# Kernel tuning notes

Hardware: AMD Instinct MI355X
Metric: run time of the kernel (lower is better)

## Reference

```python
import jax, jax.numpy as jnp
import numpy as np

N_NODES = 100000
N_EDGES = 640000
NIN = 128
NOUT = 128


def setup_inputs() -> dict:
    key = jax.random.key(0)
    ks = jax.random.split(key, 10)
    scale = 1.0 / np.sqrt(NIN)
    x = jax.random.normal(ks[0], (N_NODES, NIN), dtype=jnp.float32)
    edge_index = jax.random.randint(ks[1], (2, N_EDGES), 0, N_NODES, dtype=jnp.int64)
    edge_attr = jnp.zeros((N_EDGES, 1), dtype=jnp.float32)
    Wk = jax.random.uniform(ks[2], (NIN, NOUT), jnp.float32, -scale, scale)
    bk = jax.random.uniform(ks[3], (NOUT,), jnp.float32, -scale, scale)
    Wq = jax.random.uniform(ks[4], (NIN, NOUT), jnp.float32, -scale, scale)
    bq = jax.random.uniform(ks[5], (NOUT,), jnp.float32, -scale, scale)
    Wv = jax.random.uniform(ks[6], (NIN, NOUT), jnp.float32, -scale, scale)
    bv = jax.random.uniform(ks[7], (NOUT,), jnp.float32, -scale, scale)
    Wskip = jax.random.uniform(ks[8], (NIN, NOUT), jnp.float32, -scale, scale)
    bias = jax.random.uniform(ks[9], (NOUT,), jnp.float32, -scale, scale)
    return {
        "x": x, "edge_index": edge_index, "edge_attr": edge_attr,
        "Wk": Wk, "bk": bk, "Wq": Wq, "bq": bq,
        "Wv": Wv, "bv": bv, "Wskip": Wskip, "bias": bias,
    }


def reference(x, edge_index, edge_attr, Wk, bk, Wq, bq, Wv, bv, Wskip, bias):
    # PyG ResGatedGraphConv: out_i = W_skip x_i + b + sum_{j->i} sigmoid(k_i + q_j) * v_j
    # k = lin_key(x) (applied to dst), q = lin_query(x) (src), v = lin_value(x) (src)
    src, dst = edge_index[0], edge_index[1]
    k = x @ Wk + bk            # [N, NOUT]
    q = x @ Wq + bq            # [N, NOUT]
    v = x @ Wv + bv            # [N, NOUT]
    eta = jax.nn.sigmoid(k[dst] + q[src])   # [E, NOUT] per-edge gate
    msg = eta * v[src]                       # [E, NOUT]
    agg = jax.ops.segment_sum(msg, dst, num_segments=x.shape[0])  # [N, NOUT]
    return agg + x @ Wskip + bias
```

## Files before the change

### kernel.cpp

```cpp
#include <hip/hip_runtime.h>
#include <hip/hip_bf16.h>

typedef __bf16 v4bf __attribute__((ext_vector_type(4)));
typedef __bf16 v8bf __attribute__((ext_vector_type(8)));
typedef float  v16f __attribute__((ext_vector_type(16)));
typedef float  f4v  __attribute__((ext_vector_type(4)));
typedef unsigned int u4v __attribute__((ext_vector_type(4)));

#define LOG2E 1.44269504088896340736f

__device__ __forceinline__ unsigned short f2bf(float f) {
    union { float f; unsigned int u; } a; a.f = f;
    unsigned int r = a.u + 0x7FFFu + ((a.u >> 16) & 1u);
    return (unsigned short)(r >> 16);
}

__device__ __forceinline__ void unpack8v(u4v w, float* f) {
    #pragma unroll
    for (int i = 0; i < 4; ++i) {
        f[2 * i]     = __uint_as_float(w[i] << 16);
        f[2 * i + 1] = __uint_as_float(w[i] & 0xFFFF0000u);
    }
}

__global__ __launch_bounds__(256) void prep_w_zero(
    const float* __restrict__ Wk, const float* __restrict__ Wq,
    const float* __restrict__ Wv, const float* __restrict__ Ws,
    unsigned short* __restrict__ Wt, int* __restrict__ deg, int N)
{
    int i = blockIdx.x * 256 + threadIdx.x;
    if (i < 65536) {
        int m = i >> 14;
        int r = i & 16383;
        int n = r >> 7, k = r & 127;
        const float* W = (m == 0) ? Wk : (m == 1) ? Wq : (m == 2) ? Wv : Ws;
        float scale = (m == 0) ? -LOG2E : (m == 1) ? LOG2E : 1.0f;
        Wt[i] = f2bf(W[k * 128 + n] * scale);
    }
    if (i < N) deg[i] = 0;
}

__global__ __launch_bounds__(1024, 4) void gemm_fused(
    const float* __restrict__ x, int N,
    const unsigned short* __restrict__ Wt,
    const float* __restrict__ bk, const float* __restrict__ bq,
    const float* __restrict__ bv, const float* __restrict__ bs,
    unsigned short* __restrict__ kws, unsigned short* __restrict__ qv,
    float* __restrict__ out,
    const int* __restrict__ ei, int E,
    int* __restrict__ deg, int* __restrict__ pos)
{
    for (int e = blockIdx.x * 1024 + threadIdx.x; e < E; e += gridDim.x * 1024) {
        pos[e] = atomicAdd(&deg[ei[E + e]], 1);
    }

    __shared__ __align__(16) unsigned short xs[128 * 132];
    const int t  = threadIdx.x;
    const int tb = blockIdx.x * 128;

    {
        const int srow = t >> 3;
        const int scol = (t & 7) << 4;
        const int gr = tb + srow;
        float4 f0, f1, f2, f3;
        if (gr < N) {
            const float* xp = x + (size_t)gr * 128 + scol;
            f0 = *(const float4*)(xp);
            f1 = *(const float4*)(xp + 4);
            f2 = *(const float4*)(xp + 8);
            f3 = *(const float4*)(xp + 12);
        } else {
            f0 = f1 = f2 = f3 = make_float4(0.f, 0.f, 0.f, 0.f);
        }
        unsigned short* sp = xs + srow * 132 + scol;
        ushort4 p;
        p.x = f2bf(f0.x); p.y = f2bf(f0.y); p.z = f2bf(f0.z); p.w = f2bf(f0.w);
        *(ushort4*)(sp) = p;
        p.x = f2bf(f1.x); p.y = f2bf(f1.y); p.z = f2bf(f1.z); p.w = f2bf(f1.w);
        *(ushort4*)(sp + 4) = p;
        p.x = f2bf(f2.x); p.y = f2bf(f2.y); p.z = f2bf(f2.z); p.w = f2bf(f2.w);
        *(ushort4*)(sp + 8) = p;
        p.x = f2bf(f3.x); p.y = f2bf(f3.y); p.z = f2bf(f3.z); p.w = f2bf(f3.w);
        *(ushort4*)(sp + 12) = p;
    }

    const int wid = t >> 6;
    const int m   = wid >> 2;
    const int ct  = wid & 3;
    const int l   = t & 63;
    const int lr  = l & 31;
    const int h   = l >> 5;
    const int kb  = h * 8;

    v8bf b[8];
    {
        const unsigned short* wp = Wt + m * 16384 + (ct * 32 + lr) * 128 + kb;
        #pragma unroll
        for (int c = 0; c < 8; ++c) b[c] = *(const v8bf*)(wp + c * 16);
    }
    const float* bvec = (m == 0) ? bk : (m == 1) ? bq : (m == 2) ? bv : bs;
    const float bscale = (m == 0) ? -LOG2E : (m == 1) ? LOG2E : 1.0f;
    float4 biasg[4];
    #pragma unroll
    for (int g = 0; g < 4; ++g) {
        float4 bb = *(const float4*)(bvec + ct * 32 + 8 * g + 4 * h);
        biasg[g] = make_float4(bb.x * bscale, bb.y * bscale, bb.z * bscale, bb.w * bscale);
    }
    unsigned short* dst; int dstride;
    if (m == 0)      { dst = kws;      dstride = 128; }
    else if (m == 1) { dst = qv;       dstride = 256; }
    else             { dst = qv + 128; dstride = 256; }

    __syncthreads();

    #pragma unroll
    for (int rt = 0; rt < 4; ++rt) {
        const unsigned short* ap = xs + (rt * 32 + lr) * 132 + kb;
        v16f acc = {};
        #pragma unroll
        for (int c = 0; c < 8; ++c) {
            v4bf a0 = *(const v4bf*)(ap + c * 16);
            v4bf a1 = *(const v4bf*)(ap + c * 16 + 4);
            v8bf a = __builtin_shufflevector(a0, a1, 0, 1, 2, 3, 4, 5, 6, 7);
            acc = __builtin_amdgcn_mfma_f32_32x32x16_bf16(b[c], a, acc, 0, 0, 0);
        }
        const int row = tb + rt * 32 + lr;
        if (row < N) {
            if (m == 3) {
                float* orow = out + (size_t)row * 128 + ct * 32 + 4 * h;
                #pragma unroll
                for (int g = 0; g < 4; ++g) {
                    float4 o;
                    o.x = acc[4 * g + 0] + biasg[g].x;
                    o.y = acc[4 * g + 1] + biasg[g].y;
                    o.z = acc[4 * g + 2] + biasg[g].z;
                    o.w = acc[4 * g + 3] + biasg[g].w;
                    *(float4*)(orow + 8 * g) = o;
                }
            } else {
                unsigned short* drow = dst + (size_t)row * dstride + ct * 32 + 4 * h;
                #pragma unroll
                for (int g = 0; g < 4; ++g) {
                    ushort4 p;
                    p.x = f2bf(acc[4 * g + 0] + biasg[g].x);
                    p.y = f2bf(acc[4 * g + 1] + biasg[g].y);
                    p.z = f2bf(acc[4 * g + 2] + biasg[g].z);
                    p.w = f2bf(acc[4 * g + 3] + biasg[g].w);
                    *(ushort4*)(drow + 8 * g) = p;
                }
            }
        }
    }
}


__global__ __launch_bounds__(256) void scan_chunks(
    const int* __restrict__ deg, int N, int* __restrict__ rowStart,
    int* __restrict__ chunkTot)
{
    __shared__ int sums[256];
    const int t = threadIdx.x;
    const int base = blockIdx.x * 1024 + t * 4;
    int d0 = 0, d1 = 0, d2 = 0, d3 = 0;
    if (base + 3 < N) {
        int4 dd = *(const int4*)(deg + base);
        d0 = dd.x; d1 = dd.y; d2 = dd.z; d3 = dd.w;
    } else {
        if (base + 0 < N) d0 = deg[base + 0];
        if (base + 1 < N) d1 = deg[base + 1];
        if (base + 2 < N) d2 = deg[base + 2];
        if (base + 3 < N) d3 = deg[base + 3];
    }
    int tot = d0 + d1 + d2 + d3;
    sums[t] = tot;
    __syncthreads();
    #pragma unroll
    for (int off = 1; off < 256; off <<= 1) {
        int v = (t >= off) ? sums[t - off] : 0;
        __syncthreads();
        sums[t] += v;
        __syncthreads();
    }
    int excl = sums[t] - tot;
    if (base + 0 < N) rowStart[base + 0] = excl;
    if (base + 1 < N) rowStart[base + 1] = excl + d0;
    if (base + 2 < N) rowStart[base + 2] = excl + d0 + d1;
    if (base + 3 < N) rowStart[base + 3] = excl + d0 + d1 + d2;
    if (t == 255) chunkTot[blockIdx.x] = sums[255];
}

__global__ __launch_bounds__(256) void add_offsets(
    int* __restrict__ rowStart, const int* __restrict__ chunkTot,
    int N, int nChunks)
{
    __shared__ int s[128];
    const int t = threadIdx.x;
    if (t < 128) s[t] = (t < nChunks) ? chunkTot[t] : 0;
    __syncthreads();
    #pragma unroll
    for (int off = 1; off < 128; off <<= 1) {
        int u = 0;
        if (t < 128 && t >= off) u = s[t - off];
        __syncthreads();
        if (t < 128) s[t] += u;
        __syncthreads();
    }
    const int coff = (blockIdx.x == 0) ? 0 : s[blockIdx.x - 1];
    const int base = blockIdx.x * 1024 + t * 4;
    if (base + 3 < N) {
        int4 r = *(const int4*)(rowStart + base);
        r.x += coff; r.y += coff; r.z += coff; r.w += coff;
        *(int4*)(rowStart + base) = r;
    } else {
        #pragma unroll
        for (int j = 0; j < 4; ++j) {
            if (base + j < N) rowStart[base + j] += coff;
        }
    }
}

__global__ __launch_bounds__(256) void fill_csr(
    const int* __restrict__ ei, int E,
    const int* __restrict__ rowStart, const int* __restrict__ pos,
    int* __restrict__ elist)
{
    int e = blockIdx.x * 256 + threadIdx.x;
    if (e >= E) return;
    elist[rowStart[ei[E + e]] + pos[e]] = ei[e];
}

__global__ __launch_bounds__(256, 8) void gather_agg(
    const int* __restrict__ rowStart, const int* __restrict__ deg,
    const int* __restrict__ elist,
    const unsigned short* __restrict__ kws,
    const unsigned short* __restrict__ qv,
    float* __restrict__ out, int N)
{
    const int grp = threadIdx.x >> 4;
    const int fo  = (threadIdx.x & 15) << 3;
    const int gstride = gridDim.x * 16;
    const unsigned short* qvb = qv + fo;

    for (int node = blockIdx.x * 16 + grp; node < N; node += gstride) {
        float* orow = out + (size_t)node * 128 + fo;
        f4v o0 = *(const f4v*)(orow);
        f4v o1 = *(const f4v*)(orow + 4);
        u4v kraw = *(const u4v*)(kws + (size_t)node * 128 + fo);
        const int p0 = rowStart[node];
        const int dg = deg[node];
        const int e  = p0 + dg;
        const int eL = e - 1;

        float nkf[8];
        unpack8v(kraw, nkf);
        float acc[8] = {};

        for (int base = p0; base < e; base += 4) {
            int idx[4];
            #pragma unroll
            for (int s = 0; s < 4; ++s) {
                int pp = base + s;
                idx[s] = elist[pp < e ? pp : eL];
            }
            u4v qr[4], vr[4];
            #pragma unroll
            for (int s = 0; s < 4; ++s) {
                const unsigned short* r = qvb + (idx[s] << 8);
                qr[s] = *(const u4v*)(r);
                vr[s] = *(const u4v*)(r + 128);
            }
            #pragma unroll
            for (int s = 0; s < 4; ++s) {
                u4v vv = vr[s];
                if (base + s >= e) { vv[0] = 0u; vv[1] = 0u; vv[2] = 0u; vv[3] = 0u; }
                float qf[8], vf[8];
                unpack8v(qr[s], qf);
                unpack8v(vv, vf);
                #pragma unroll
                for (int j = 0; j < 8; ++j) {
                    float ex = __builtin_amdgcn_exp2f(nkf[j] - qf[j]);
                    acc[j] = fmaf(__builtin_amdgcn_rcpf(1.0f + ex), vf[j], acc[j]);
                }
            }
        }

        o0[0] += acc[0]; o0[1] += acc[1]; o0[2] += acc[2]; o0[3] += acc[3];
        o1[0] += acc[4]; o1[1] += acc[5]; o1[2] += acc[6]; o1[3] += acc[7];
        *(f4v*)(orow)     = o0;
        *(f4v*)(orow + 4) = o1;
    }
}

extern "C" void kernel_launch(void* const* d_in, const int* in_sizes, int n_in,
                              void* d_out, int out_size, void* d_ws, size_t ws_size,
                              hipStream_t stream) {
    const float* x    = (const float*)d_in[0];
    const int*   ei   = (const int*)d_in[1];
    const float* Wk   = (const float*)d_in[3];
    const float* bk   = (const float*)d_in[4];
    const float* Wq   = (const float*)d_in[5];
    const float* bq   = (const float*)d_in[6];
    const float* Wv   = (const float*)d_in[7];
    const float* bv   = (const float*)d_in[8];
    const float* Ws   = (const float*)d_in[9];
    const float* bias = (const float*)d_in[10];

    const int N = in_sizes[0] / 128;
    const int E = in_sizes[1] / 2;
    float* out = (float*)d_out;

    unsigned short* kws = (unsigned short*)d_ws;
    unsigned short* qv  = kws + (size_t)N * 128;
    int* deg      = (int*)(qv + (size_t)N * 256);
    int* rowStart = deg + N;
    int* chunkTot = rowStart + N;
    int* pos      = chunkTot + 128;
    int* elist    = pos + E;
    unsigned short* Wt = (unsigned short*)(elist + E);

    const int nChunks = (N + 1023) / 1024;
    const int ntiles128 = (N + 127) >> 7;

    prep_w_zero<<<512, 256, 0, stream>>>(Wk, Wq, Wv, Ws, Wt, deg, N);
    gemm_fused<<<ntiles128, 1024, 0, stream>>>(
        x, N, Wt, bk, bq, bv, bias, kws, qv, out, ei, E, deg, pos);

    scan_chunks<<<nChunks, 256, 0, stream>>>(deg, N, rowStart, chunkTot);
    add_offsets<<<nChunks, 256, 0, stream>>>(rowStart, chunkTot, N, nChunks);
    fill_csr<<<(E + 255) / 256, 256, 0, stream>>>(ei, E, rowStart, pos, elist);

    gather_agg<<<2048, 256, 0, stream>>>(
        rowStart, deg, elist, kws, qv, out, N);
}
```

Before: 304.5 us.

## Shrink GEMM tiles to 32 rows per block and launch one gather thread-group per node

The fused GEMM now uses 256-thread blocks that each handle 32 rows. Each wave keeps the A fragments in registers and streams the four 32-column weight tiles from global memory, where before it held one weight tile and looped over four row tiles. This gives four times as many smaller blocks with less shared memory, for better occupancy and load balance, but weights are reloaded per block and bias is loaded per column tile. The gather kernel drops its grid-stride loop and launches one 16-thread group per node with a lower occupancy hint, trading persistent scheduling for a larger grid.

Result: faster. 298.5 us (-2.0%).

```diff
diff --git a/kernel.cpp b/kernel.cpp
--- a/kernel.cpp
+++ b/kernel.cpp
@@ -40,7 +40,7 @@
     if (i < N) deg[i] = 0;
 }
 
-__global__ __launch_bounds__(1024, 4) void gemm_fused(
+__global__ __launch_bounds__(256, 4) void gemm_fused(
     const float* __restrict__ x, int N,
     const unsigned short* __restrict__ Wt,
     const float* __restrict__ bk, const float* __restrict__ bq,
@@ -50,13 +50,13 @@
     const int* __restrict__ ei, int E,
     int* __restrict__ deg, int* __restrict__ pos)
 {
-    for (int e = blockIdx.x * 1024 + threadIdx.x; e < E; e += gridDim.x * 1024) {
+    for (int e = blockIdx.x * 256 + threadIdx.x; e < E; e += gridDim.x * 256) {
         pos[e] = atomicAdd(&deg[ei[E + e]], 1);
     }
 
-    __shared__ __align__(16) unsigned short xs[128 * 132];
+    __shared__ __align__(16) unsigned short xs[32 * 132];
     const int t  = threadIdx.x;
-    const int tb = blockIdx.x * 128;
+    const int tb = blockIdx.x * 32;
 
     {
         const int srow = t >> 3;
@@ -84,28 +84,14 @@
         *(ushort4*)(sp + 12) = p;
     }
 
-    const int wid = t >> 6;
-    const int m   = wid >> 2;
-    const int ct  = wid & 3;
-    const int l   = t & 63;
-    const int lr  = l & 31;
-    const int h   = l >> 5;
-    const int kb  = h * 8;
-
-    v8bf b[8];
-    {
-        const unsigned short* wp = Wt + m * 16384 + (ct * 32 + lr) * 128 + kb;
-        #pragma unroll
-        for (int c = 0; c < 8; ++c) b[c] = *(const v8bf*)(wp + c * 16);
-    }
+    const int m  = t >> 6;
+    const int l  = t & 63;
+    const int lr = l & 31;
+    const int h  = l >> 5;
+    const int kb = h * 8;
+
     const float* bvec = (m == 0) ? bk : (m == 1) ? bq : (m == 2) ? bv : bs;
     const float bscale = (m == 0) ? -LOG2E : (m == 1) ? LOG2E : 1.0f;
-    float4 biasg[4];
-    #pragma unroll
-    for (int g = 0; g < 4; ++g) {
-        float4 bb = *(const float4*)(bvec + ct * 32 + 8 * g + 4 * h);
-        biasg[g] = make_float4(bb.x * bscale, bb.y * bscale, bb.z * bscale, bb.w * bscale);
-    }
     unsigned short* dst; int dstride;
     if (m == 0)      { dst = kws;      dstride = 128; }
     else if (m == 1) { dst = qv;       dstride = 256; }
@@ -113,39 +99,54 @@
 
     __syncthreads();
 
-    #pragma unroll
-    for (int rt = 0; rt < 4; ++rt) {
-        const unsigned short* ap = xs + (rt * 32 + lr) * 132 + kb;
-        v16f acc = {};
+    v8bf a[8];
+    {
+        const unsigned short* ap = xs + lr * 132 + kb;
         #pragma unroll
         for (int c = 0; c < 8; ++c) {
             v4bf a0 = *(const v4bf*)(ap + c * 16);
             v4bf a1 = *(const v4bf*)(ap + c * 16 + 4);
-            v8bf a = __builtin_shufflevector(a0, a1, 0, 1, 2, 3, 4, 5, 6, 7);
-            acc = __builtin_amdgcn_mfma_f32_32x32x16_bf16(b[c], a, acc, 0, 0, 0);
-        }
-        const int row = tb + rt * 32 + lr;
+            a[c] = __builtin_shufflevector(a0, a1, 0, 1, 2, 3, 4, 5, 6, 7);
+        }
+    }
+
+    const int row = tb + lr;
+
+    #pragma unroll
+    for (int ct = 0; ct < 4; ++ct) {
+        v8bf b[8];
+        const unsigned short* wp = Wt + m * 16384 + (ct * 32 + lr) * 128 + kb;
+        #pragma unroll
+        for (int c = 0; c < 8; ++c) b[c] = *(const v8bf*)(wp + c * 16);
+
+        v16f acc = {};
+        #pragma unroll
+        for (int c = 0; c < 8; ++c)
+            acc = __builtin_amdgcn_mfma_f32_32x32x16_bf16(b[c], a[c], acc, 0, 0, 0);
+
         if (row < N) {
             if (m == 3) {
                 float* orow = out + (size_t)row * 128 + ct * 32 + 4 * h;
                 #pragma unroll
                 for (int g = 0; g < 4; ++g) {
+                    float4 bb = *(const float4*)(bvec + ct * 32 + 8 * g + 4 * h);
                     float4 o;
-                    o.x = acc[4 * g + 0] + biasg[g].x;
-                    o.y = acc[4 * g + 1] + biasg[g].y;
-                    o.z = acc[4 * g + 2] + biasg[g].z;
-                    o.w = acc[4 * g + 3] + biasg[g].w;
+                    o.x = acc[4 * g + 0] + bb.x;
+                    o.y = acc[4 * g + 1] + bb.y;
+                    o.z = acc[4 * g + 2] + bb.z;
+                    o.w = acc[4 * g + 3] + bb.w;
                     *(float4*)(orow + 8 * g) = o;
                 }
             } else {
                 unsigned short* drow = dst + (size_t)row * dstride + ct * 32 + 4 * h;
                 #pragma unroll
                 for (int g = 0; g < 4; ++g) {
+                    float4 bb = *(const float4*)(bvec + ct * 32 + 8 * g + 4 * h);
                     ushort4 p;
-                    p.x = f2bf(acc[4 * g + 0] + biasg[g].x);
-                    p.y = f2bf(acc[4 * g + 1] + biasg[g].y);
-                    p.z = f2bf(acc[4 * g + 2] + biasg[g].z);
-                    p.w = f2bf(acc[4 * g + 3] + biasg[g].w);
+                    p.x = f2bf(acc[4 * g + 0] + bb.x * bscale);
+                    p.y = f2bf(acc[4 * g + 1] + bb.y * bscale);
+                    p.z = f2bf(acc[4 * g + 2] + bb.z * bscale);
+                    p.w = f2bf(acc[4 * g + 3] + bb.w * bscale);
                     *(ushort4*)(drow + 8 * g) = p;
                 }
             }
@@ -229,66 +230,66 @@
     elist[rowStart[ei[E + e]] + pos[e]] = ei[e];
 }
 
-__global__ __launch_bounds__(256, 8) void gather_agg(
+__global__ __launch_bounds__(256, 4) void gather_agg(
     const int* __restrict__ rowStart, const int* __restrict__ deg,
     const int* __restrict__ elist,
     const unsigned short* __restrict__ kws,
     const unsigned short* __restrict__ qv,
     float* __restrict__ out, int N)
 {
-    const int grp = threadIdx.x >> 4;
-    const int fo  = (threadIdx.x & 15) << 3;
-    const int gstride = gridDim.x * 16;
+    int gid = blockIdx.x * 256 + threadIdx.x;
+    int node = gid >> 4;
+    if (node >= N) return;
+    const int fo = (gid & 15) << 3;
+
+    float* orow = out + (size_t)node * 128 + fo;
+    f4v o0 = *(const f4v*)(orow);
+    f4v o1 = *(const f4v*)(orow + 4);
+    u4v kraw = *(const u4v*)(kws + (size_t)node * 128 + fo);
+    const int p0 = rowStart[node];
+    const int dg = deg[node];
+    const int e  = p0 + dg;
+    const int eL = e - 1;
+
+    float nkf[8];
+    unpack8v(kraw, nkf);
+    float acc[8] = {};
+
     const unsigned short* qvb = qv + fo;
 
-    for (int node = blockIdx.x * 16 + grp; node < N; node += gstride) {
-        float* orow = out + (size_t)node * 128 + fo;
-        f4v o0 = *(const f4v*)(orow);
-        f4v o1 = *(const f4v*)(orow + 4);
-        u4v kraw = *(const u4v*)(kws + (size_t)node * 128 + fo);
-        const int p0 = rowStart[node];
-        const int dg = deg[node];
-        const int e  = p0 + dg;
-        const int eL = e - 1;
-
-        float nkf[8];
-        unpack8v(kraw, nkf);
-        float acc[8] = {};
-
-        for (int base = p0; base < e; base += 4) {
-            int idx[4];
+    for (int base = p0; base < e; base += 4) {
+        int idx[4];
+        #pragma unroll
+        for (int s = 0; s < 4; ++s) {
+            int pp = base + s;
+            idx[s] = elist[pp < e ? pp : eL];
+        }
+        u4v qr[4], vr[4];
+        #pragma unroll
+        for (int s = 0; s < 4; ++s) {
+            const unsigned short* r = qvb + (idx[s] << 8);
+            qr[s] = *(const u4v*)(r);
+            vr[s] = *(const u4v*)(r + 128);
+        }
+        #pragma unroll
+        for (int s = 0; s < 4; ++s) {
+            u4v vv = vr[s];
+            if (base + s >= e) { vv[0] = 0u; vv[1] = 0u; vv[2] = 0u; vv[3] = 0u; }
+            float qf[8], vf[8];
+            unpack8v(qr[s], qf);
+            unpack8v(vv, vf);
             #pragma unroll
-            for (int s = 0; s < 4; ++s) {
-                int pp = base + s;
-                idx[s] = elist[pp < e ? pp : eL];
+            for (int j = 0; j < 8; ++j) {
+                float ex = __builtin_amdgcn_exp2f(nkf[j] - qf[j]);
+                acc[j] = fmaf(__builtin_amdgcn_rcpf(1.0f + ex), vf[j], acc[j]);
             }
-            u4v qr[4], vr[4];
-            #pragma unroll
-            for (int s = 0; s < 4; ++s) {
-                const unsigned short* r = qvb + (idx[s] << 8);
-                qr[s] = *(const u4v*)(r);
-                vr[s] = *(const u4v*)(r + 128);
-            }
-            #pragma unroll
-            for (int s = 0; s < 4; ++s) {
-                u4v vv = vr[s];
-                if (base + s >= e) { vv[0] = 0u; vv[1] = 0u; vv[2] = 0u; vv[3] = 0u; }
-                float qf[8], vf[8];
-                unpack8v(qr[s], qf);
-                unpack8v(vv, vf);
-                #pragma unroll
-                for (int j = 0; j < 8; ++j) {
-                    float ex = __builtin_amdgcn_exp2f(nkf[j] - qf[j]);
-                    acc[j] = fmaf(__builtin_amdgcn_rcpf(1.0f + ex), vf[j], acc[j]);
-                }
-            }
-        }
-
-        o0[0] += acc[0]; o0[1] += acc[1]; o0[2] += acc[2]; o0[3] += acc[3];
-        o1[0] += acc[4]; o1[1] += acc[5]; o1[2] += acc[6]; o1[3] += acc[7];
-        *(f4v*)(orow)     = o0;
-        *(f4v*)(orow + 4) = o1;
-    }
+        }
+    }
+
+    o0[0] += acc[0]; o0[1] += acc[1]; o0[2] += acc[2]; o0[3] += acc[3];
+    o1[0] += acc[4]; o1[1] += acc[5]; o1[2] += acc[6]; o1[3] += acc[7];
+    *(f4v*)(orow)     = o0;
+    *(f4v*)(orow + 4) = o1;
 }
 
 extern "C" void kernel_launch(void* const* d_in, const int* in_sizes, int n_in,
@@ -319,16 +320,16 @@
     unsigned short* Wt = (unsigned short*)(elist + E);
 
     const int nChunks = (N + 1023) / 1024;
-    const int ntiles128 = (N + 127) >> 7;
+    const int ntiles32 = (N + 31) >> 5;
 
     prep_w_zero<<<512, 256, 0, stream>>>(Wk, Wq, Wv, Ws, Wt, deg, N);
-    gemm_fused<<<ntiles128, 1024, 0, stream>>>(
+    gemm_fused<<<ntiles32, 256, 0, stream>>>(
         x, N, Wt, bk, bq, bv, bias, kws, qv, out, ei, E, deg, pos);
 
     scan_chunks<<<nChunks, 256, 0, stream>>>(deg, N, rowStart, chunkTot);
     add_offsets<<<nChunks, 256, 0, stream>>>(rowStart, chunkTot, N, nChunks);
     fill_csr<<<(E + 255) / 256, 256, 0, stream>>>(ei, E, rowStart, pos, elist);
 
-    gather_agg<<<2048, 256, 0, stream>>>(
+    gather_agg<<<((size_t)N * 16 + 255) / 256, 256, 0, stream>>>(
         rowStart, deg, elist, kws, qv, out, N);
 }
```
